# Optimization experiments

Measured on AMD Instinct MI355X. Metric: run time of the kernel, lower is better.

## Reference

```python
import jax, jax.numpy as jnp
import numpy as np

# Constants (consts in the original repo)
B, H, W, D, R = 4, 384, 512, 256, 4
H8, W8 = H // 8, W // 8

# Diamond displacement set: y in [-r, r], x in [|y|-r, r-|y|]  -> len = 2r^2+2r+1 = 41
def _disps():
    ys, xs = [], []
    for y in range(-R, R + 1):
        for x in range(abs(y) - R, R - abs(y) + 1):
            ys.append(y); xs.append(x)
    return np.asarray(ys, np.float32), np.asarray(xs, np.float32)
YS_NP, XS_NP = _disps()
L = YS_NP.shape[0]  # 41


def setup_inputs() -> dict:
    key = jax.random.key(0)
    k1, k2, k3 = jax.random.split(key, 3)
    return {
        "feat1": jax.random.normal(k1, (B, D, H8, W8), dtype=jnp.float32),
        "feat2": jax.random.normal(k2, (B, D, H8, W8), dtype=jnp.float32),
        "curr_flow": jax.random.normal(k3, (2, H8, W8), dtype=jnp.float32),
    }


def _pool(corr, s):
    # average-pool last two dims of (B, H8, W8, hk, wk) by factor s
    if s == 1:
        return corr
    b, h, w, hk, wk = corr.shape
    return corr.reshape(b, h, w, hk // s, s, wk // s, s).mean(axis=(4, 6))


def _sample_level(corr_k, curr_flow, k):
    # corr_k: (B, H8, W8, hk, wk); bilinear grid_sample (align_corners=True, zeros padding)
    hk, wk = corr_k.shape[3], corr_k.shape[4]
    sc = 2.0 ** k
    hn, wn = H / sc, W / sc  # faithful to source: normalizes by full-res H/2^k, W/2^k
    ii = jnp.arange(H8, dtype=jnp.float32)[:, None, None]   # (H8,1,1)
    jj = jnp.arange(W8, dtype=jnp.float32)[None, :, None]   # (1,W8,1)
    ys = jnp.asarray(YS_NP); xs = jnp.asarray(XS_NP)        # (L,)
    fx = curr_flow[1][:, :, None]  # (H8,W8,1)
    fy = curr_flow[0][:, :, None]
    gx = (jj / sc + fx / sc + xs) / (wn / 2.0) - 1.0         # (H8,W8,L) normalized x
    gy = (ii / sc + fy / sc + ys) / (hn / 2.0) - 1.0         # (H8,W8,L) normalized y
    # align_corners=True: [-1,1] -> [0, size-1]
    px = (gx + 1.0) * 0.5 * (wk - 1)
    py = (gy + 1.0) * 0.5 * (hk - 1)
    x0 = jnp.floor(px); y0 = jnp.floor(py)
    tx = px - x0; ty = py - y0
    x0i = x0.astype(jnp.int32); y0i = y0.astype(jnp.int32)
    flat = corr_k.reshape(B, H8, W8, hk * wk)

    def gather(yi, xi):
        inb = ((yi >= 0) & (yi < hk) & (xi >= 0) & (xi < wk)).astype(flat.dtype)
        yc = jnp.clip(yi, 0, hk - 1); xc = jnp.clip(xi, 0, wk - 1)
        idx = jnp.broadcast_to((yc * wk + xc)[None], (B, H8, W8, L))
        return jnp.take_along_axis(flat, idx, axis=3) * inb[None]

    v00 = gather(y0i, x0i)
    v01 = gather(y0i, x0i + 1)
    v10 = gather(y0i + 1, x0i)
    v11 = gather(y0i + 1, x0i + 1)
    out = (v00 * (1 - tx) * (1 - ty) + v01 * tx * (1 - ty)
           + v10 * (1 - tx) * ty + v11 * tx * ty)        # (B,H8,W8,L)
    return jnp.transpose(out, (0, 3, 1, 2))               # (B,L,H8,W8)


def reference(feat1, feat2, curr_flow):
    # all-pairs correlation volume: (B, H8, W8, H8, W8)
    corr = jnp.einsum('bdij,bdkl->bijkl', feat1, feat2) / jnp.sqrt(jnp.float32(D))
    levels = [_sample_level(_pool(corr, 2 ** k), curr_flow, k) for k in range(4)]
    return jnp.stack(levels, axis=2)  # (B, L, 4, H8, W8)
```

## Files before the change

### kernel.cpp

```cpp
#include <hip/hip_runtime.h>

#define H8    48
#define W8    64
#define SPAT  3072
#define NL    41

#define W0c 12
#define H0c 10
#define W1c 7
#define H1c 6
#define W2c 4
#define H2c 4
#define W3c 3
#define H3c 3

__constant__ float c_ys[NL] = {
    -4,
    -3,-3,-3,
    -2,-2,-2,-2,-2,
    -1,-1,-1,-1,-1,-1,-1,
     0, 0, 0, 0, 0, 0, 0, 0, 0,
     1, 1, 1, 1, 1, 1, 1,
     2, 2, 2, 2, 2,
     3, 3, 3,
     4
};
__constant__ float c_xs[NL] = {
     0,
    -1, 0, 1,
    -2,-1, 0, 1, 2,
    -3,-2,-1, 0, 1, 2, 3,
    -4,-3,-2,-1, 0, 1, 2, 3, 4,
    -3,-2,-1, 0, 1, 2, 3,
    -2,-1, 0, 1, 2,
    -1, 0, 1,
     0
};

__global__ __launch_bounds__(256) void pool_kernel(
        const float* __restrict__ feat2,
        float* __restrict__ L0, float* __restrict__ L1,
        float* __restrict__ L2, float* __restrict__ L3) {
    int bid = blockIdx.x;
    int b = bid >> 3;
    int s = bid & 7;
    int ch = threadIdx.x;
    const float* src = feat2 + (size_t)(b * 256 + ch) * SPAT;

    if (s < 2) {
        for (int y = s * 5; y < s * 5 + 5; ++y)
            #pragma unroll
            for (int xq = 0; xq < 3; ++xq) {
                float4 v = *(const float4*)(src + y * W8 + xq * 4);
                float* d = L0 + ((size_t)(b * H0c + y) * W0c + xq * 4) * 256 + ch;
                d[0] = v.x; d[256] = v.y; d[512] = v.z; d[768] = v.w;
            }
    } else if (s < 4) {
        for (int y = (s - 2) * 3; y < (s - 2) * 3 + 3; ++y)
            #pragma unroll
            for (int x = 0; x < W1c; ++x) {
                const float* p = src + (y * 2) * W8 + x * 2;
                float v = (p[0] + p[1] + p[W8] + p[W8 + 1]) * 0.25f;
                L1[((size_t)(b * H1c + y) * W1c + x) * 256 + ch] = v;
            }
    } else if (s == 4) {
        #pragma unroll
        for (int y = 0; y < H2c; ++y)
            #pragma unroll
            for (int x = 0; x < W2c; ++x) {
                const float* p = src + (y * 4) * W8 + x * 4;
                float acc = 0.f;
                #pragma unroll
                for (int rr = 0; rr < 4; ++rr) {
                    float4 v = *(const float4*)(p + rr * W8);
                    acc += v.x + v.y + v.z + v.w;
                }
                L2[((size_t)(b * H2c + y) * W2c + x) * 256 + ch] = acc * 0.0625f;
            }
    } else {
        int y = s - 5;
        #pragma unroll
        for (int x = 0; x < W3c; ++x) {
            const float* p = src + (y * 8) * W8 + x * 8;
            float acc = 0.f;
            #pragma unroll
            for (int rr = 0; rr < 8; ++rr) {
                float4 v0 = *(const float4*)(p + rr * W8);
                float4 v1 = *(const float4*)(p + rr * W8 + 4);
                acc += v0.x + v0.y + v0.z + v0.w + v1.x + v1.y + v1.z + v1.w;
            }
            L3[((size_t)(b * H3c + y) * W3c + x) * 256 + ch] = acc * 0.015625f;
        }
    }
}

__global__ __launch_bounds__(256) void lookup_kernel(
        const float* __restrict__ feat1,
        const float* __restrict__ L0, const float* __restrict__ L1,
        const float* __restrict__ L2, const float* __restrict__ L3,
        const float* __restrict__ flow, float* __restrict__ out) {
    __shared__ float f1s[8 * 260];
    __shared__ float dots[4][8][9];
    __shared__ float rawx[8], rawy[8];
    __shared__ int   mx0[4][8], my0[4][8];

    int bid = blockIdx.x;
    int b  = bid / 384;
    int r  = bid % 384;
    int i  = r >> 3;
    int jg = r & 7;
    int j0 = jg * 8;
    int tid = threadIdx.x;

    {
        const float* p = feat1 + ((size_t)(b * 256 + tid) * H8 + i) * W8 + j0;
        float4 a = *(const float4*)p;
        float4 c = *(const float4*)(p + 4);
        f1s[0*260 + tid] = a.x; f1s[1*260 + tid] = a.y;
        f1s[2*260 + tid] = a.z; f1s[3*260 + tid] = a.w;
        f1s[4*260 + tid] = c.x; f1s[5*260 + tid] = c.y;
        f1s[6*260 + tid] = c.z; f1s[7*260 + tid] = c.w;
    }
    __syncthreads();

    int k    = tid >> 6;
    int lane = tid & 63;
    int p = lane >> 3;
    int l = lane & 7;
    int j = j0 + p;

    const float* f2k; int Wc, Hc;
    if (k == 0)      { f2k = L0 + (size_t)b * H0c * W0c * 256; Wc = W0c; Hc = H0c; }
    else if (k == 1) { f2k = L1 + (size_t)b * H1c * W1c * 256; Wc = W1c; Hc = H1c; }
    else if (k == 2) { f2k = L2 + (size_t)b * H2c * W2c * 256; Wc = W2c; Hc = H2c; }
    else             { f2k = L3 + (size_t)b * H3c * W3c * 256; Wc = W3c; Hc = H3c; }

    int wt = W8 >> k, ht = H8 >> k;
    float inv_sc = 1.0f / (float)(1 << k);
    float rx = (float)(wt - 1) / (512.0f * inv_sc);
    float ry = (float)(ht - 1) / (384.0f * inv_sc);

    float fy = flow[i * W8 + j];
    float fx = flow[SPAT + i * W8 + j];
    float base_x = ((float)j + fx) * inv_sc;
    float base_y = ((float)i + fy) * inv_sc;
    int x0lo = (int)floorf((base_x - 4.0f) * rx);
    int y0lo = (int)floorf((base_y - 4.0f) * ry);

    float4 f1r[8];
    #pragma unroll
    for (int m = 0; m < 8; ++m)
        f1r[m] = *(const float4*)&f1s[p * 260 + (m * 8 + l) * 4];

    #pragma unroll
    for (int cy = 0; cy < 3; ++cy) {
        int y = y0lo + cy;
        #pragma unroll
        for (int cx = 0; cx < 3; ++cx) {
            int x = x0lo + cx;
            float acc = 0.0f;
            if (y >= 0 && y < Hc && x >= 0 && x < Wc) {
                const float* f2p = f2k + ((size_t)(y * Wc + x)) * 256 + l * 4;
                #pragma unroll
                for (int m = 0; m < 8; ++m) {
                    const float4 v = *(const float4*)(f2p + m * 32);
                    acc += v.x * f1r[m].x + v.y * f1r[m].y
                         + v.z * f1r[m].z + v.w * f1r[m].w;
                }
            }
            acc += __shfl_xor(acc, 1, 64);
            acc += __shfl_xor(acc, 2, 64);
            acc += __shfl_xor(acc, 4, 64);
            if (l == 0) dots[k][p][cy * 3 + cx] = acc;
        }
    }
    if (l == 0) {
        mx0[k][p] = x0lo;
        my0[k][p] = y0lo;
        if (k == 0) { rawx[p] = (float)j + fx; rawy[p] = (float)i + fy; }
    }
    __syncthreads();

    for (int t = tid; t < NL * 4 * 8; t += 256) {
        int p2 = t & 7;
        int lk = t >> 3;
        int kk = lk & 3;
        int ld = lk >> 2;
        float sc2 = (float)(1 << kk);
        float rx2 = (float)((W8 >> kk) - 1) / (512.0f / sc2);
        float ry2 = (float)((H8 >> kk) - 1) / (384.0f / sc2);
        float bx = rawx[p2] / sc2;
        float by = rawy[p2] / sc2;
        float px = (bx + c_xs[ld]) * rx2;
        float py = (by + c_ys[ld]) * ry2;
        float x0f = floorf(px), y0f = floorf(py);
        float tx = px - x0f, ty = py - y0f;
        int cx0 = (int)x0f - mx0[kk][p2];
        int cy0 = (int)y0f - my0[kk][p2];
        const float* dp = &dots[kk][p2][cy0 * 3 + cx0];
        float d00 = dp[0], d01 = dp[1], d10 = dp[3], d11 = dp[4];
        float v = d00 * (1.0f - tx) * (1.0f - ty) + d01 * tx * (1.0f - ty)
                + d10 * (1.0f - tx) * ty          + d11 * tx * ty;
        out[(size_t)((b * NL + ld) * 4 + kk) * SPAT + i * W8 + j0 + p2] = v * 0.0625f;
    }
}

extern "C" void kernel_launch(void* const* d_in, const int* in_sizes, int n_in,
                              void* d_out, int out_size, void* d_ws, size_t ws_size,
                              hipStream_t stream) {
    const float* feat1 = (const float*)d_in[0];
    const float* feat2 = (const float*)d_in[1];
    const float* flow  = (const float*)d_in[2];
    float* out = (float*)d_out;
    float* ws  = (float*)d_ws;

    float* L0 = ws;
    float* L1 = L0 + 4 * H0c * W0c * 256;
    float* L2 = L1 + 4 * H1c * W1c * 256;
    float* L3 = L2 + 4 * H2c * W2c * 256;

    hipLaunchKernelGGL(pool_kernel, dim3(32), dim3(256), 0, stream,
                       feat2, L0, L1, L2, L3);
    hipLaunchKernelGGL(lookup_kernel, dim3(1536), dim3(256), 0, stream,
                       feat1, L0, L1, L2, L3, flow, out);
}
```

Baseline: 45.22 us.

## Spread pooling over more blocks and precompute level scale constants

```diff
diff --git a/kernel.cpp b/kernel.cpp
--- a/kernel.cpp
+++ b/kernel.cpp
@@ -37,60 +37,81 @@
      0
 };
 
+__constant__ float c_rx[4] = {63.0f/512.0f, 62.0f/512.0f, 60.0f/512.0f, 56.0f/512.0f};
+__constant__ float c_ry[4] = {47.0f/384.0f, 46.0f/384.0f, 44.0f/384.0f, 40.0f/384.0f};
+__constant__ float c_isc[4] = {1.0f, 0.5f, 0.25f, 0.125f};
+
 __global__ __launch_bounds__(256) void pool_kernel(
         const float* __restrict__ feat2,
         float* __restrict__ L0, float* __restrict__ L1,
         float* __restrict__ L2, float* __restrict__ L3) {
     int bid = blockIdx.x;
-    int b = bid >> 3;
-    int s = bid & 7;
+    int b = bid / 23;
+    int s = bid % 23;
     int ch = threadIdx.x;
     const float* src = feat2 + (size_t)(b * 256 + ch) * SPAT;
 
-    if (s < 2) {
-        for (int y = s * 5; y < s * 5 + 5; ++y)
+    if (s < 10) {
+        int y = s;
+        #pragma unroll
+        for (int xq = 0; xq < 3; ++xq) {
+            float4 v = *(const float4*)(src + y * W8 + xq * 4);
+            float* d = L0 + ((size_t)(b * H0c + y) * W0c + xq * 4) * 256 + ch;
+            d[0] = v.x; d[256] = v.y; d[512] = v.z; d[768] = v.w;
+        }
+    } else if (s < 16) {
+        int y = s - 10;
+        const float* p0 = src + (y * 2) * W8;
+        const float* p1 = p0 + W8;
+        float rowsum[16];
+        #pragma unroll
+        for (int q = 0; q < 4; ++q) {
+            float4 a = *(const float4*)(p0 + q * 4);
+            float4 c = *(const float4*)(p1 + q * 4);
+            rowsum[q*4+0] = a.x + c.x; rowsum[q*4+1] = a.y + c.y;
+            rowsum[q*4+2] = a.z + c.z; rowsum[q*4+3] = a.w + c.w;
+        }
+        float* d = L1 + ((size_t)(b * H1c + y) * W1c) * 256 + ch;
+        #pragma unroll
+        for (int x = 0; x < W1c; ++x)
+            d[(size_t)x * 256] = (rowsum[2*x] + rowsum[2*x+1]) * 0.25f;
+    } else if (s < 20) {
+        int y = s - 16;
+        float colsum[16];
+        #pragma unroll
+        for (int c = 0; c < 16; ++c) colsum[c] = 0.f;
+        #pragma unroll
+        for (int rr = 0; rr < 4; ++rr) {
+            const float* p = src + (y * 4 + rr) * W8;
             #pragma unroll
-            for (int xq = 0; xq < 3; ++xq) {
-                float4 v = *(const float4*)(src + y * W8 + xq * 4);
-                float* d = L0 + ((size_t)(b * H0c + y) * W0c + xq * 4) * 256 + ch;
-                d[0] = v.x; d[256] = v.y; d[512] = v.z; d[768] = v.w;
+            for (int q = 0; q < 4; ++q) {
+                float4 v = *(const float4*)(p + q * 4);
+                colsum[q*4+0] += v.x; colsum[q*4+1] += v.y;
+                colsum[q*4+2] += v.z; colsum[q*4+3] += v.w;
             }
-    } else if (s < 4) {
-        for (int y = (s - 2) * 3; y < (s - 2) * 3 + 3; ++y)
+        }
+        float* d = L2 + ((size_t)(b * H2c + y) * W2c) * 256 + ch;
+        #pragma unroll
+        for (int x = 0; x < W2c; ++x)
+            d[(size_t)x * 256] = (colsum[4*x] + colsum[4*x+1]
+                                + colsum[4*x+2] + colsum[4*x+3]) * 0.0625f;
+    } else {
+        int y = s - 20;
+        float cell[3] = {0.f, 0.f, 0.f};
+        #pragma unroll
+        for (int rr = 0; rr < 8; ++rr) {
+            const float* p = src + (y * 8 + rr) * W8;
             #pragma unroll
-            for (int x = 0; x < W1c; ++x) {
-                const float* p = src + (y * 2) * W8 + x * 2;
-                float v = (p[0] + p[1] + p[W8] + p[W8 + 1]) * 0.25f;
-                L1[((size_t)(b * H1c + y) * W1c + x) * 256 + ch] = v;
+            for (int x = 0; x < 3; ++x) {
+                float4 v0 = *(const float4*)(p + x * 8);
+                float4 v1 = *(const float4*)(p + x * 8 + 4);
+                cell[x] += v0.x + v0.y + v0.z + v0.w + v1.x + v1.y + v1.z + v1.w;
             }
-    } else if (s == 4) {
-        #pragma unroll
-        for (int y = 0; y < H2c; ++y)
-            #pragma unroll
-            for (int x = 0; x < W2c; ++x) {
-                const float* p = src + (y * 4) * W8 + x * 4;
-                float acc = 0.f;
-                #pragma unroll
-                for (int rr = 0; rr < 4; ++rr) {
-                    float4 v = *(const float4*)(p + rr * W8);
-                    acc += v.x + v.y + v.z + v.w;
-                }
-                L2[((size_t)(b * H2c + y) * W2c + x) * 256 + ch] = acc * 0.0625f;
-            }
-    } else {
-        int y = s - 5;
-        #pragma unroll
-        for (int x = 0; x < W3c; ++x) {
-            const float* p = src + (y * 8) * W8 + x * 8;
-            float acc = 0.f;
-            #pragma unroll
-            for (int rr = 0; rr < 8; ++rr) {
-                float4 v0 = *(const float4*)(p + rr * W8);
-                float4 v1 = *(const float4*)(p + rr * W8 + 4);
-                acc += v0.x + v0.y + v0.z + v0.w + v1.x + v1.y + v1.z + v1.w;
-            }
-            L3[((size_t)(b * H3c + y) * W3c + x) * 256 + ch] = acc * 0.015625f;
-        }
+        }
+        float* d = L3 + ((size_t)(b * H3c + y) * W3c) * 256 + ch;
+        #pragma unroll
+        for (int x = 0; x < 3; ++x)
+            d[(size_t)x * 256] = cell[x] * 0.015625f;
     }
 }
 
@@ -135,10 +156,7 @@
     else if (k == 2) { f2k = L2 + (size_t)b * H2c * W2c * 256; Wc = W2c; Hc = H2c; }
     else             { f2k = L3 + (size_t)b * H3c * W3c * 256; Wc = W3c; Hc = H3c; }
 
-    int wt = W8 >> k, ht = H8 >> k;
-    float inv_sc = 1.0f / (float)(1 << k);
-    float rx = (float)(wt - 1) / (512.0f * inv_sc);
-    float ry = (float)(ht - 1) / (384.0f * inv_sc);
+    float rx = c_rx[k], ry = c_ry[k], inv_sc = c_isc[k];
 
     float fy = flow[i * W8 + j];
     float fx = flow[SPAT + i * W8 + j];
@@ -186,13 +204,11 @@
         int lk = t >> 3;
         int kk = lk & 3;
         int ld = lk >> 2;
-        float sc2 = (float)(1 << kk);
-        float rx2 = (float)((W8 >> kk) - 1) / (512.0f / sc2);
-        float ry2 = (float)((H8 >> kk) - 1) / (384.0f / sc2);
-        float bx = rawx[p2] / sc2;
-        float by = rawy[p2] / sc2;
-        float px = (bx + c_xs[ld]) * rx2;
-        float py = (by + c_ys[ld]) * ry2;
+        float isc2 = c_isc[kk];
+        float rx2 = c_rx[kk];
+        float ry2 = c_ry[kk];
+        float px = (rawx[p2] * isc2 + c_xs[ld]) * rx2;
+        float py = (rawy[p2] * isc2 + c_ys[ld]) * ry2;
         float x0f = floorf(px), y0f = floorf(py);
         float tx = px - x0f, ty = py - y0f;
         int cx0 = (int)x0f - mx0[kk][p2];
@@ -219,7 +235,7 @@
     float* L2 = L1 + 4 * H1c * W1c * 256;
     float* L3 = L2 + 4 * H2c * W2c * 256;
 
-    hipLaunchKernelGGL(pool_kernel, dim3(32), dim3(256), 0, stream,
+    hipLaunchKernelGGL(pool_kernel, dim3(92), dim3(256), 0, stream,
                        feat2, L0, L1, L2, L3);
     hipLaunchKernelGGL(lookup_kernel, dim3(1536), dim3(256), 0, stream,
                        feat1, L0, L1, L2, L3, flow, out);
```

New measurement: 41.12 us. 9.1% less time.
